# Kernel tuning notes

Hardware: AMD Instinct MI355X
Metric: run time of the kernel (lower is better)

## Reference

```python
import jax, jax.numpy as jnp
import numpy as np


def _butter1(Wn, highpass):
    """First-order Butterworth digital coefficients (bilinear transform),
    matching scipy.signal.butter(1, Wn, btype). Wn is nyquist-normalized."""
    K = jnp.tan(jnp.pi * Wn / 2.0)
    a1 = (K - 1.0) / (K + 1.0)
    if highpass:
        b0 = 1.0 / (K + 1.0)
        b1 = -b0
    else:
        b0 = K / (K + 1.0)
        b1 = b0
    return b0, b1, a1


def setup_inputs() -> dict:
    key = jax.random.key(0)
    B, T = 128, 262144
    x = jax.random.normal(key, (B, T), dtype=jnp.float32)
    return {
        "x": x,
        "center_freq": jnp.float32(1000.0),  # nn.Parameter
        "bandwidth": jnp.float32(500.0),     # nn.Parameter
        "gain": jnp.float32(1.0),            # nn.Parameter
        "sample_rate": 48000,
    }


def reference(x, center_freq, bandwidth, gain, sample_rate):
    nyq = sample_rate / 2.0
    low_wn = (center_freq - bandwidth / 2.0) / nyq
    high_wn = (center_freq + bandwidth / 2.0) / nyq
    # cascaded 1st-order highpass(low_wn) then lowpass(high_wn) = bandpass
    bh0, bh1, ah1 = _butter1(low_wn, highpass=True)
    bl0, bl1, al1 = _butter1(high_wn, highpass=False)

    xt = x.T  # [T, B] -- scan over time, vectorized over batch
    zeros = jnp.zeros((x.shape[0],), dtype=x.dtype)

    def step(carry, x_t):
        x_prev, y1_prev, y2_prev = carry
        y1 = bh0 * x_t + bh1 * x_prev - ah1 * y1_prev   # highpass stage
        y2 = bl0 * y1 + bl1 * y1_prev - al1 * y2_prev   # lowpass stage
        return (x_t, y1, y2), y2

    _, yt = jax.lax.scan(step, (zeros, zeros, zeros), xt)
    return yt.T * gain  # [B, T]
```

## Files before the change

kernel.cpp:

```cpp
#include <hip/hip_runtime.h>
#include <math.h>

#define B_    128
#define T_    262144
#define L_    16
#define NT_   256
#define WCH_  16
#define OT_   (NT_ * L_)
#define TPR_  (T_ / OT_)
#define NW_   (NT_ / 64)
#define STR_  (L_ + 1)

typedef float f32x4 __attribute__((ext_vector_type(4)));

struct Coef {
    float bh0, bh1;
    float p, q, r;
    float blc0, blc1;
};

__device__ inline void iir_step(const Coef& c, float xt, float& x_prev,
                                float& y1, float& y2) {
    float c1 = fmaf(c.bh0,  xt, c.bh1  * x_prev);
    float cx = fmaf(c.blc0, xt, c.blc1 * x_prev);
    float ny1 = fmaf(c.p, y1, c1);
    float ny2 = fmaf(c.q, y1, fmaf(c.r, y2, cx));
    y1 = ny1; y2 = ny2; x_prev = xt;
}

struct Mat { float p, q, r; };
__device__ inline Mat mat_sq(Mat m) {
    Mat o; o.p = m.p * m.p; o.q = m.q * (m.p + m.r); o.r = m.r * m.r; return o;
}
__device__ inline Mat mat_mul(Mat a, Mat b) {
    Mat o; o.p = a.p * b.p; o.q = fmaf(a.q, b.p, a.r * b.q); o.r = a.r * b.r;
    return o;
}
__device__ inline float2 mat_apply_add(Mat m, float2 v, float2 add) {
    float2 o;
    o.x = fmaf(m.p, v.x, add.x);
    o.y = fmaf(m.q, v.x, fmaf(m.r, v.y, add.y));
    return o;
}

__global__ __launch_bounds__(NT_, 8) void bp_kernel(
        const float* __restrict__ x, float* __restrict__ out,
        const float* __restrict__ cfp, const float* __restrict__ bwp,
        const float* __restrict__ gp, const int* __restrict__ srp) {
    __shared__ float  ys[NT_ * STR_];
    __shared__ float2 wagg[WCH_];
    __shared__ float2 wsagg[NW_];

    const int blk  = blockIdx.x;
    const int row  = blk >> 6;
    const int ti   = blk & (TPR_ - 1);
    const int t    = threadIdx.x;
    const int lane = t & 63;
    const int wav  = t >> 6;
    const long tile_start = (long)row * T_ + (long)ti * OT_;
    const float* xb = x + tile_start;

    const f32x4* xg = (const f32x4*)(xb + t * L_);
    f32x4 v0 = xg[0], v1 = xg[1], v2 = xg[2], v3 = xg[3];
    f32x4 w0 = (f32x4)(0.f), w1 = w0, w2 = w0, w3 = w0;
    if (t < WCH_ && ti != 0) {
        const f32x4* wg = (const f32x4*)(xb - WCH_ * L_ + t * L_);
        w0 = wg[0]; w1 = wg[1]; w2 = wg[2]; w3 = wg[3];
    }
    float xp = __shfl_up(v3.w, 1u, 64);
    if (lane == 0) xp = (ti != 0 || t != 0) ? xb[t * L_ - 1] : 0.f;

    Coef cf;
    {
        const float PIH = 1.57079632679489661923f;
        float cfv = *cfp, bwv = *bwp;
        float nyq = 0.5f * (float)(*srp);
        float K1 = tanf(PIH * (cfv - 0.5f * bwv) / nyq);
        float K2 = tanf(PIH * (cfv + 0.5f * bwv) / nyq);
        float inv1 = 1.0f / (K1 + 1.0f);
        float ah1 = (K1 - 1.0f) * inv1;
        float inv2 = 1.0f / (K2 + 1.0f);
        float bl0 = K2 * inv2;
        float al1 = (K2 - 1.0f) * inv2;
        cf.bh0 = inv1;
        cf.bh1 = -inv1;
        cf.p = -ah1;
        cf.q = bl0 - bl0 * ah1;
        cf.r = -al1;
        cf.blc0 = bl0 * inv1;
        cf.blc1 = -bl0 * inv1;
    }
    const float gain = *gp;

    Mat A  = { cf.p, cf.q, cf.r };
    Mat AL = A;
    #pragma unroll
    for (int k = 0; k < 4; ++k) AL = mat_sq(AL);
    Mat R = { 1.f, 0.f, 1.f };
    {
        Mat Mp = AL;
        unsigned b = (unsigned)lane;
        #pragma unroll
        for (int k = 0; k < 6; ++k) {
            if (b & 1u) R = mat_mul(Mp, R);
            b >>= 1u;
            if (k < 5) Mp = mat_sq(Mp);
        }
    }

    float xa[L_];
    xa[0]=v0.x; xa[1]=v0.y; xa[2]=v0.z; xa[3]=v0.w;
    xa[4]=v1.x; xa[5]=v1.y; xa[6]=v1.z; xa[7]=v1.w;
    xa[8]=v2.x; xa[9]=v2.y; xa[10]=v2.z; xa[11]=v2.w;
    xa[12]=v3.x; xa[13]=v3.y; xa[14]=v3.z; xa[15]=v3.w;
    float y2l[L_];
    float y1 = 0.f, y2 = 0.f;
    {
        float xprev = xp;
        #pragma unroll
        for (int i = 0; i < L_; ++i) {
            iir_step(cf, xa[i], xprev, y1, y2);
            y2l[i] = y2;
        }
    }

    float wxp = __shfl_up(w3.w, 1u, 64);
    if (t < WCH_) {
        float wa[L_];
        wa[0]=w0.x; wa[1]=w0.y; wa[2]=w0.z; wa[3]=w0.w;
        wa[4]=w1.x; wa[5]=w1.y; wa[6]=w1.z; wa[7]=w1.w;
        wa[8]=w2.x; wa[9]=w2.y; wa[10]=w2.z; wa[11]=w2.w;
        wa[12]=w3.x; wa[13]=w3.y; wa[14]=w3.z; wa[15]=w3.w;
        float wy1 = 0.f, wy2 = 0.f;
        float wp = (t == 0) ? 0.f : wxp;
        #pragma unroll
        for (int i = 0; i < L_; ++i) iir_step(cf, wa[i], wp, wy1, wy2);
        wagg[t] = make_float2(wy1, wy2);
    }

    float2 a = make_float2(y1, y2);
    Mat Pw = AL;
    #pragma unroll
    for (int o = 1; o < 64; o <<= 1) {
        float vx = __shfl_up(a.x, (unsigned)o, 64);
        float vy = __shfl_up(a.y, (unsigned)o, 64);
        if (lane >= o) {
            a.y = fmaf(Pw.q, vx, fmaf(Pw.r, vy, a.y));
            a.x = fmaf(Pw.p, vx, a.x);
        }
        Pw = mat_sq(Pw);
    }
    float2 ex;
    ex.x = __shfl_up(a.x, 1u, 64);
    ex.y = __shfl_up(a.y, 1u, 64);
    if (lane == 0) { ex.x = 0.f; ex.y = 0.f; }
    if (lane == 63) wsagg[wav] = a;
    __syncthreads();

    float2 S = make_float2(0.f, 0.f);
    #pragma unroll
    for (int j = 0; j < WCH_; ++j) S = mat_apply_add(AL, S, wagg[j]);
    #pragma unroll
    for (int u = 0; u < NW_ - 1; ++u)
        if (wav > u) S = mat_apply_add(Pw, S, wsagg[u]);

    float2 E = mat_apply_add(R, S, ex);

    {
        float c1 = E.x, c2 = E.y;
        float* cp = ys + t * STR_;
        #pragma unroll
        for (int i = 0; i < L_; ++i) {
            float nc1 = cf.p * c1;
            float nc2 = fmaf(cf.q, c1, cf.r * c2);
            c1 = nc1; c2 = nc2;
            cp[i] = (y2l[i] + c2) * gain;
        }
    }
    __syncthreads();

    f32x4* og = (f32x4*)(out + tile_start);
    #pragma unroll
    for (int k = 0; k < 4; ++k) {
        int F = t + NT_ * k;
        int chunk = F >> 2, pos = 4 * (F & 3);
        const float* p = ys + chunk * STR_ + pos;
        f32x4 o; o.x = p[0]; o.y = p[1]; o.z = p[2]; o.w = p[3];
        __builtin_nontemporal_store(o, og + F);
    }
}

extern "C" void kernel_launch(void* const* d_in, const int* in_sizes, int n_in,
                              void* d_out, int out_size, void* d_ws, size_t ws_size,
                              hipStream_t stream) {
    const float* x   = (const float*)d_in[0];
    const float* cfp = (const float*)d_in[1];
    const float* bwp = (const float*)d_in[2];
    const float* gp  = (const float*)d_in[3];
    const int*   srp = (const int*)d_in[4];
    float* out = (float*)d_out;

    dim3 blk(NT_), grd(B_ * TPR_);
    bp_kernel<<<grd, blk, 0, stream>>>(x, out, cfp, bwp, gp, srp);
}
```

Measured before the change: 239.1 us.

## Process two batch rows per block to interleave independent recurrences

Each block now handles the same time tile for two adjacent rows, interleaving the two independent scan chains: the serial per-thread IIR, the wave scan shuffles and the carry fix-up. This amortises per-block setup such as coefficient computation and the matrix powers, and exposes instruction-level parallelism. The cost is double the registers and LDS per block, half the grid size and a lower occupancy hint (launch bounds 8 to 4), which can reduce latency hiding for the memory-bound loads and stores.

```diff
diff --git a/kernel.cpp b/kernel.cpp
--- a/kernel.cpp
+++ b/kernel.cpp
@@ -43,32 +43,42 @@
     return o;
 }
 
-__global__ __launch_bounds__(NT_, 8) void bp_kernel(
+__global__ __launch_bounds__(NT_, 4) void bp_kernel(
         const float* __restrict__ x, float* __restrict__ out,
         const float* __restrict__ cfp, const float* __restrict__ bwp,
         const float* __restrict__ gp, const int* __restrict__ srp) {
-    __shared__ float  ys[NT_ * STR_];
-    __shared__ float2 wagg[WCH_];
-    __shared__ float2 wsagg[NW_];
+    __shared__ float  ys[2][NT_ * STR_];
+    __shared__ float2 wagg[2][WCH_];
+    __shared__ float2 wsagg[2][NW_];
 
     const int blk  = blockIdx.x;
-    const int row  = blk >> 6;
+    const int pr   = blk >> 6;
     const int ti   = blk & (TPR_ - 1);
     const int t    = threadIdx.x;
     const int lane = t & 63;
     const int wav  = t >> 6;
-    const long tile_start = (long)row * T_ + (long)ti * OT_;
-    const float* xb = x + tile_start;
-
-    const f32x4* xg = (const f32x4*)(xb + t * L_);
-    f32x4 v0 = xg[0], v1 = xg[1], v2 = xg[2], v3 = xg[3];
+    const long baseA = (long)(2 * pr)     * T_ + (long)ti * OT_;
+    const long baseB = (long)(2 * pr + 1) * T_ + (long)ti * OT_;
+    const float* xA = x + baseA;
+    const float* xB = x + baseB;
+
+    const f32x4* xgA = (const f32x4*)(xA + t * L_);
+    const f32x4* xgB = (const f32x4*)(xB + t * L_);
+    f32x4 vA0 = xgA[0], vA1 = xgA[1], vA2 = xgA[2], vA3 = xgA[3];
+    f32x4 vB0 = xgB[0], vB1 = xgB[1], vB2 = xgB[2], vB3 = xgB[3];
     f32x4 w0 = (f32x4)(0.f), w1 = w0, w2 = w0, w3 = w0;
-    if (t < WCH_ && ti != 0) {
-        const f32x4* wg = (const f32x4*)(xb - WCH_ * L_ + t * L_);
+    const int wt = t & 15;
+    if (t < 32 && ti != 0) {
+        const float* wb = (t < 16 ? xA : xB) - WCH_ * L_ + wt * L_;
+        const f32x4* wg = (const f32x4*)wb;
         w0 = wg[0]; w1 = wg[1]; w2 = wg[2]; w3 = wg[3];
     }
-    float xp = __shfl_up(v3.w, 1u, 64);
-    if (lane == 0) xp = (ti != 0 || t != 0) ? xb[t * L_ - 1] : 0.f;
+    float xpA = __shfl_up(vA3.w, 1u, 64);
+    float xpB = __shfl_up(vB3.w, 1u, 64);
+    if (lane == 0) {
+        xpA = (ti != 0 || t != 0) ? xA[t * L_ - 1] : 0.f;
+        xpB = (ti != 0 || t != 0) ? xB[t * L_ - 1] : 0.f;
+    }
 
     Coef cf;
     {
@@ -108,85 +118,114 @@
         }
     }
 
-    float xa[L_];
-    xa[0]=v0.x; xa[1]=v0.y; xa[2]=v0.z; xa[3]=v0.w;
-    xa[4]=v1.x; xa[5]=v1.y; xa[6]=v1.z; xa[7]=v1.w;
-    xa[8]=v2.x; xa[9]=v2.y; xa[10]=v2.z; xa[11]=v2.w;
-    xa[12]=v3.x; xa[13]=v3.y; xa[14]=v3.z; xa[15]=v3.w;
-    float y2l[L_];
-    float y1 = 0.f, y2 = 0.f;
-    {
-        float xprev = xp;
+    float aA_[L_], aB_[L_];
+    aA_[0]=vA0.x; aA_[1]=vA0.y; aA_[2]=vA0.z; aA_[3]=vA0.w;
+    aA_[4]=vA1.x; aA_[5]=vA1.y; aA_[6]=vA1.z; aA_[7]=vA1.w;
+    aA_[8]=vA2.x; aA_[9]=vA2.y; aA_[10]=vA2.z; aA_[11]=vA2.w;
+    aA_[12]=vA3.x; aA_[13]=vA3.y; aA_[14]=vA3.z; aA_[15]=vA3.w;
+    aB_[0]=vB0.x; aB_[1]=vB0.y; aB_[2]=vB0.z; aB_[3]=vB0.w;
+    aB_[4]=vB1.x; aB_[5]=vB1.y; aB_[6]=vB1.z; aB_[7]=vB1.w;
+    aB_[8]=vB2.x; aB_[9]=vB2.y; aB_[10]=vB2.z; aB_[11]=vB2.w;
+    aB_[12]=vB3.x; aB_[13]=vB3.y; aB_[14]=vB3.z; aB_[15]=vB3.w;
+    float y2lA[L_], y2lB[L_];
+    float y1A = 0.f, y2A = 0.f, y1B = 0.f, y2B = 0.f;
+    {
+        float xprevA = xpA, xprevB = xpB;
         #pragma unroll
         for (int i = 0; i < L_; ++i) {
-            iir_step(cf, xa[i], xprev, y1, y2);
-            y2l[i] = y2;
+            iir_step(cf, aA_[i], xprevA, y1A, y2A);
+            iir_step(cf, aB_[i], xprevB, y1B, y2B);
+            y2lA[i] = y2A;
+            y2lB[i] = y2B;
         }
     }
 
     float wxp = __shfl_up(w3.w, 1u, 64);
-    if (t < WCH_) {
+    if (t < 32) {
         float wa[L_];
         wa[0]=w0.x; wa[1]=w0.y; wa[2]=w0.z; wa[3]=w0.w;
         wa[4]=w1.x; wa[5]=w1.y; wa[6]=w1.z; wa[7]=w1.w;
         wa[8]=w2.x; wa[9]=w2.y; wa[10]=w2.z; wa[11]=w2.w;
         wa[12]=w3.x; wa[13]=w3.y; wa[14]=w3.z; wa[15]=w3.w;
         float wy1 = 0.f, wy2 = 0.f;
-        float wp = (t == 0) ? 0.f : wxp;
+        float wp = (wt == 0) ? 0.f : wxp;
         #pragma unroll
         for (int i = 0; i < L_; ++i) iir_step(cf, wa[i], wp, wy1, wy2);
-        wagg[t] = make_float2(wy1, wy2);
-    }
-
-    float2 a = make_float2(y1, y2);
+        wagg[t >> 4][wt] = make_float2(wy1, wy2);
+    }
+
+    float2 aA = make_float2(y1A, y2A);
+    float2 aB = make_float2(y1B, y2B);
     Mat Pw = AL;
     #pragma unroll
     for (int o = 1; o < 64; o <<= 1) {
-        float vx = __shfl_up(a.x, (unsigned)o, 64);
-        float vy = __shfl_up(a.y, (unsigned)o, 64);
+        float vxA = __shfl_up(aA.x, (unsigned)o, 64);
+        float vyA = __shfl_up(aA.y, (unsigned)o, 64);
+        float vxB = __shfl_up(aB.x, (unsigned)o, 64);
+        float vyB = __shfl_up(aB.y, (unsigned)o, 64);
         if (lane >= o) {
-            a.y = fmaf(Pw.q, vx, fmaf(Pw.r, vy, a.y));
-            a.x = fmaf(Pw.p, vx, a.x);
+            aA.y = fmaf(Pw.q, vxA, fmaf(Pw.r, vyA, aA.y));
+            aA.x = fmaf(Pw.p, vxA, aA.x);
+            aB.y = fmaf(Pw.q, vxB, fmaf(Pw.r, vyB, aB.y));
+            aB.x = fmaf(Pw.p, vxB, aB.x);
         }
         Pw = mat_sq(Pw);
     }
-    float2 ex;
-    ex.x = __shfl_up(a.x, 1u, 64);
-    ex.y = __shfl_up(a.y, 1u, 64);
-    if (lane == 0) { ex.x = 0.f; ex.y = 0.f; }
-    if (lane == 63) wsagg[wav] = a;
+    float2 exA, exB;
+    exA.x = __shfl_up(aA.x, 1u, 64);
+    exA.y = __shfl_up(aA.y, 1u, 64);
+    exB.x = __shfl_up(aB.x, 1u, 64);
+    exB.y = __shfl_up(aB.y, 1u, 64);
+    if (lane == 0) { exA.x = exA.y = exB.x = exB.y = 0.f; }
+    if (lane == 63) { wsagg[0][wav] = aA; wsagg[1][wav] = aB; }
     __syncthreads();
 
-    float2 S = make_float2(0.f, 0.f);
-    #pragma unroll
-    for (int j = 0; j < WCH_; ++j) S = mat_apply_add(AL, S, wagg[j]);
-    #pragma unroll
-    for (int u = 0; u < NW_ - 1; ++u)
-        if (wav > u) S = mat_apply_add(Pw, S, wsagg[u]);
-
-    float2 E = mat_apply_add(R, S, ex);
-
-    {
-        float c1 = E.x, c2 = E.y;
-        float* cp = ys + t * STR_;
+    float2 SA = make_float2(0.f, 0.f), SB = SA;
+    #pragma unroll
+    for (int j = 0; j < WCH_; ++j) {
+        SA = mat_apply_add(AL, SA, wagg[0][j]);
+        SB = mat_apply_add(AL, SB, wagg[1][j]);
+    }
+    #pragma unroll
+    for (int u = 0; u < NW_ - 1; ++u) {
+        if (wav > u) {
+            SA = mat_apply_add(Pw, SA, wsagg[0][u]);
+            SB = mat_apply_add(Pw, SB, wsagg[1][u]);
+        }
+    }
+
+    float2 EA = mat_apply_add(R, SA, exA);
+    float2 EB = mat_apply_add(R, SB, exB);
+
+    {
+        float c1A = EA.x, c2A = EA.y, c1B = EB.x, c2B = EB.y;
+        float* cpA = ys[0] + t * STR_;
+        float* cpB = ys[1] + t * STR_;
         #pragma unroll
         for (int i = 0; i < L_; ++i) {
-            float nc1 = cf.p * c1;
-            float nc2 = fmaf(cf.q, c1, cf.r * c2);
-            c1 = nc1; c2 = nc2;
-            cp[i] = (y2l[i] + c2) * gain;
+            float n1A = cf.p * c1A;
+            float n2A = fmaf(cf.q, c1A, cf.r * c2A);
+            float n1B = cf.p * c1B;
+            float n2B = fmaf(cf.q, c1B, cf.r * c2B);
+            c1A = n1A; c2A = n2A; c1B = n1B; c2B = n2B;
+            cpA[i] = (y2lA[i] + c2A) * gain;
+            cpB[i] = (y2lB[i] + c2B) * gain;
         }
     }
     __syncthreads();
 
-    f32x4* og = (f32x4*)(out + tile_start);
+    f32x4* ogA = (f32x4*)(out + baseA);
+    f32x4* ogB = (f32x4*)(out + baseB);
     #pragma unroll
     for (int k = 0; k < 4; ++k) {
         int F = t + NT_ * k;
         int chunk = F >> 2, pos = 4 * (F & 3);
-        const float* p = ys + chunk * STR_ + pos;
-        f32x4 o; o.x = p[0]; o.y = p[1]; o.z = p[2]; o.w = p[3];
-        __builtin_nontemporal_store(o, og + F);
+        const float* pA = ys[0] + chunk * STR_ + pos;
+        const float* pB = ys[1] + chunk * STR_ + pos;
+        f32x4 oA; oA.x = pA[0]; oA.y = pA[1]; oA.z = pA[2]; oA.w = pA[3];
+        f32x4 oB; oB.x = pB[0]; oB.y = pB[1]; oB.z = pB[2]; oB.w = pB[3];
+        __builtin_nontemporal_store(oA, ogA + F);
+        __builtin_nontemporal_store(oB, ogB + F);
     }
 }
 
@@ -200,6 +239,6 @@
     const int*   srp = (const int*)d_in[4];
     float* out = (float*)d_out;
 
-    dim3 blk(NT_), grd(B_ * TPR_);
+    dim3 blk(NT_), grd((B_ / 2) * TPR_);
     bp_kernel<<<grd, blk, 0, stream>>>(x, out, cfp, bwp, gp, srp);
 }
```

After: 239.6 us. No clear change (+0.2%).

## Process four consecutive tiles per block with carried state and prefetch

Applied to the files above, without the earlier changes.

Each block now handles four consecutive tiles of a row. The inter-tile state is carried exactly across tiles, so only the first tile pays for the warm-up window recompute. The next tile's input is prefetched with nontemporal loads while the current tile's scan runs. The grid shrinks fourfold and launch bounds drop to 4 waves per SIMD. Fewer blocks and serial tiles per block reduce parallelism, and the prefetch raises register pressure.

```diff
diff --git a/kernel.cpp b/kernel.cpp
--- a/kernel.cpp
+++ b/kernel.cpp
@@ -10,6 +10,8 @@
 #define TPR_  (T_ / OT_)
 #define NW_   (NT_ / 64)
 #define STR_  (L_ + 1)
+#define GPB_  4
+#define NBLK_ ((B_ * TPR_) / GPB_)
 
 typedef float f32x4 __attribute__((ext_vector_type(4)));
 
@@ -43,7 +45,7 @@
     return o;
 }
 
-__global__ __launch_bounds__(NT_, 8) void bp_kernel(
+__global__ __launch_bounds__(NT_, 4) void bp_kernel(
         const float* __restrict__ x, float* __restrict__ out,
         const float* __restrict__ cfp, const float* __restrict__ bwp,
         const float* __restrict__ gp, const int* __restrict__ srp) {
@@ -52,23 +54,32 @@
     __shared__ float2 wsagg[NW_];
 
     const int blk  = blockIdx.x;
-    const int row  = blk >> 6;
-    const int ti   = blk & (TPR_ - 1);
     const int t    = threadIdx.x;
     const int lane = t & 63;
     const int wav  = t >> 6;
-    const long tile_start = (long)row * T_ + (long)ti * OT_;
-    const float* xb = x + tile_start;
-
-    const f32x4* xg = (const f32x4*)(xb + t * L_);
-    f32x4 v0 = xg[0], v1 = xg[1], v2 = xg[2], v3 = xg[3];
+
+    const int tid0 = blk * GPB_;
+    const int row  = tid0 >> 6;
+    const int ti0  = tid0 & (TPR_ - 1);
+    const long base0 = (long)row * T_ + (long)ti0 * OT_;
+
+    {
+        const float* xb = x + base0;
+        (void)xb;
+    }
+    const float* xb0 = x + base0;
+    const f32x4* xg0 = (const f32x4*)(xb0 + t * L_);
+    f32x4 v0 = __builtin_nontemporal_load(xg0 + 0);
+    f32x4 v1 = __builtin_nontemporal_load(xg0 + 1);
+    f32x4 v2 = __builtin_nontemporal_load(xg0 + 2);
+    f32x4 v3 = __builtin_nontemporal_load(xg0 + 3);
     f32x4 w0 = (f32x4)(0.f), w1 = w0, w2 = w0, w3 = w0;
-    if (t < WCH_ && ti != 0) {
-        const f32x4* wg = (const f32x4*)(xb - WCH_ * L_ + t * L_);
+    if (t < WCH_ && ti0 != 0) {
+        const f32x4* wg = (const f32x4*)(xb0 - WCH_ * L_ + t * L_);
         w0 = wg[0]; w1 = wg[1]; w2 = wg[2]; w3 = wg[3];
     }
-    float xp = __shfl_up(v3.w, 1u, 64);
-    if (lane == 0) xp = (ti != 0 || t != 0) ? xb[t * L_ - 1] : 0.f;
+    float lxp = 0.f;
+    if (lane == 0 && (ti0 != 0 || t != 0)) lxp = xb0[t * L_ - 1];
 
     Coef cf;
     {
@@ -108,85 +119,122 @@
         }
     }
 
-    float xa[L_];
-    xa[0]=v0.x; xa[1]=v0.y; xa[2]=v0.z; xa[3]=v0.w;
-    xa[4]=v1.x; xa[5]=v1.y; xa[6]=v1.z; xa[7]=v1.w;
-    xa[8]=v2.x; xa[9]=v2.y; xa[10]=v2.z; xa[11]=v2.w;
-    xa[12]=v3.x; xa[13]=v3.y; xa[14]=v3.z; xa[15]=v3.w;
-    float y2l[L_];
-    float y1 = 0.f, y2 = 0.f;
-    {
-        float xprev = xp;
-        #pragma unroll
-        for (int i = 0; i < L_; ++i) {
-            iir_step(cf, xa[i], xprev, y1, y2);
-            y2l[i] = y2;
-        }
-    }
-
-    float wxp = __shfl_up(w3.w, 1u, 64);
-    if (t < WCH_) {
-        float wa[L_];
-        wa[0]=w0.x; wa[1]=w0.y; wa[2]=w0.z; wa[3]=w0.w;
-        wa[4]=w1.x; wa[5]=w1.y; wa[6]=w1.z; wa[7]=w1.w;
-        wa[8]=w2.x; wa[9]=w2.y; wa[10]=w2.z; wa[11]=w2.w;
-        wa[12]=w3.x; wa[13]=w3.y; wa[14]=w3.z; wa[15]=w3.w;
-        float wy1 = 0.f, wy2 = 0.f;
-        float wp = (t == 0) ? 0.f : wxp;
-        #pragma unroll
-        for (int i = 0; i < L_; ++i) iir_step(cf, wa[i], wp, wy1, wy2);
-        wagg[t] = make_float2(wy1, wy2);
-    }
-
-    float2 a = make_float2(y1, y2);
-    Mat Pw = AL;
+    float2 Scar = make_float2(0.f, 0.f);
+
     #pragma unroll
-    for (int o = 1; o < 64; o <<= 1) {
-        float vx = __shfl_up(a.x, (unsigned)o, 64);
-        float vy = __shfl_up(a.y, (unsigned)o, 64);
-        if (lane >= o) {
-            a.y = fmaf(Pw.q, vx, fmaf(Pw.r, vy, a.y));
-            a.x = fmaf(Pw.p, vx, a.x);
-        }
-        Pw = mat_sq(Pw);
-    }
-    float2 ex;
-    ex.x = __shfl_up(a.x, 1u, 64);
-    ex.y = __shfl_up(a.y, 1u, 64);
-    if (lane == 0) { ex.x = 0.f; ex.y = 0.f; }
-    if (lane == 63) wsagg[wav] = a;
-    __syncthreads();
-
-    float2 S = make_float2(0.f, 0.f);
-    #pragma unroll
-    for (int j = 0; j < WCH_; ++j) S = mat_apply_add(AL, S, wagg[j]);
-    #pragma unroll
-    for (int u = 0; u < NW_ - 1; ++u)
-        if (wav > u) S = mat_apply_add(Pw, S, wsagg[u]);
-
-    float2 E = mat_apply_add(R, S, ex);
-
-    {
-        float c1 = E.x, c2 = E.y;
-        float* cp = ys + t * STR_;
-        #pragma unroll
-        for (int i = 0; i < L_; ++i) {
-            float nc1 = cf.p * c1;
-            float nc2 = fmaf(cf.q, c1, cf.r * c2);
-            c1 = nc1; c2 = nc2;
-            cp[i] = (y2l[i] + c2) * gain;
-        }
-    }
-    __syncthreads();
-
-    f32x4* og = (f32x4*)(out + tile_start);
-    #pragma unroll
-    for (int k = 0; k < 4; ++k) {
-        int F = t + NT_ * k;
-        int chunk = F >> 2, pos = 4 * (F & 3);
-        const float* p = ys + chunk * STR_ + pos;
-        f32x4 o; o.x = p[0]; o.y = p[1]; o.z = p[2]; o.w = p[3];
-        __builtin_nontemporal_store(o, og + F);
+    for (int g = 0; g < GPB_; ++g) {
+        const long base = base0 + (long)g * OT_;
+
+        float xp = __shfl_up(v3.w, 1u, 64);
+        if (lane == 0) xp = lxp;
+
+        float xa[L_];
+        xa[0]=v0.x; xa[1]=v0.y; xa[2]=v0.z; xa[3]=v0.w;
+        xa[4]=v1.x; xa[5]=v1.y; xa[6]=v1.z; xa[7]=v1.w;
+        xa[8]=v2.x; xa[9]=v2.y; xa[10]=v2.z; xa[11]=v2.w;
+        xa[12]=v3.x; xa[13]=v3.y; xa[14]=v3.z; xa[15]=v3.w;
+        float y2l[L_];
+        float y1 = 0.f, y2 = 0.f;
+        {
+            float xprev = xp;
+            #pragma unroll
+            for (int i = 0; i < L_; ++i) {
+                iir_step(cf, xa[i], xprev, y1, y2);
+                y2l[i] = y2;
+            }
+        }
+
+        if (g == 0) {
+            float wxp = __shfl_up(w3.w, 1u, 64);
+            if (t < WCH_) {
+                float wa[L_];
+                wa[0]=w0.x; wa[1]=w0.y; wa[2]=w0.z; wa[3]=w0.w;
+                wa[4]=w1.x; wa[5]=w1.y; wa[6]=w1.z; wa[7]=w1.w;
+                wa[8]=w2.x; wa[9]=w2.y; wa[10]=w2.z; wa[11]=w2.w;
+                wa[12]=w3.x; wa[13]=w3.y; wa[14]=w3.z; wa[15]=w3.w;
+                float wy1 = 0.f, wy2 = 0.f;
+                float wp = (t == 0) ? 0.f : wxp;
+                #pragma unroll
+                for (int i = 0; i < L_; ++i) iir_step(cf, wa[i], wp, wy1, wy2);
+                wagg[t] = make_float2(wy1, wy2);
+            }
+        }
+
+        if (g + 1 < GPB_) {
+            const float* nxb = x + base + OT_;
+            const f32x4* nxg = (const f32x4*)(nxb + t * L_);
+            v0 = __builtin_nontemporal_load(nxg + 0);
+            v1 = __builtin_nontemporal_load(nxg + 1);
+            v2 = __builtin_nontemporal_load(nxg + 2);
+            v3 = __builtin_nontemporal_load(nxg + 3);
+            if (lane == 0) lxp = nxb[t * L_ - 1];
+        }
+
+        float2 a = make_float2(y1, y2);
+        Mat Pw = AL;
+        #pragma unroll
+        for (int o = 1; o < 64; o <<= 1) {
+            float vx = __shfl_up(a.x, (unsigned)o, 64);
+            float vy = __shfl_up(a.y, (unsigned)o, 64);
+            if (lane >= o) {
+                a.y = fmaf(Pw.q, vx, fmaf(Pw.r, vy, a.y));
+                a.x = fmaf(Pw.p, vx, a.x);
+            }
+            Pw = mat_sq(Pw);
+        }
+        float2 ex;
+        ex.x = __shfl_up(a.x, 1u, 64);
+        ex.y = __shfl_up(a.y, 1u, 64);
+        if (lane == 0) { ex.x = 0.f; ex.y = 0.f; }
+        if (lane == 63) wsagg[wav] = a;
+        __syncthreads();
+
+        float2 S;
+        if (g == 0) {
+            S = make_float2(0.f, 0.f);
+            #pragma unroll
+            for (int j = 0; j < WCH_; ++j) S = mat_apply_add(AL, S, wagg[j]);
+        } else {
+            S = Scar;
+        }
+
+        {
+            float2 Stot = wsagg[0];
+            #pragma unroll
+            for (int u = 1; u < NW_; ++u) Stot = mat_apply_add(Pw, Stot, wsagg[u]);
+            Mat P2 = mat_sq(Pw);
+            Mat P4 = mat_sq(P2);
+            Scar = mat_apply_add(P4, S, Stot);
+        }
+
+        float2 Sw = S;
+        #pragma unroll
+        for (int u = 0; u < NW_ - 1; ++u)
+            if (wav > u) Sw = mat_apply_add(Pw, Sw, wsagg[u]);
+        float2 E = mat_apply_add(R, Sw, ex);
+
+        {
+            float c1 = E.x, c2 = E.y;
+            float* cp = ys + t * STR_;
+            #pragma unroll
+            for (int i = 0; i < L_; ++i) {
+                float nc1 = cf.p * c1;
+                float nc2 = fmaf(cf.q, c1, cf.r * c2);
+                c1 = nc1; c2 = nc2;
+                cp[i] = (y2l[i] + c2) * gain;
+            }
+        }
+        __syncthreads();
+
+        f32x4* og = (f32x4*)(out + base);
+        #pragma unroll
+        for (int k = 0; k < 4; ++k) {
+            int F = t + NT_ * k;
+            int chunk = F >> 2, pos = 4 * (F & 3);
+            const float* p = ys + chunk * STR_ + pos;
+            f32x4 o; o.x = p[0]; o.y = p[1]; o.z = p[2]; o.w = p[3];
+            __builtin_nontemporal_store(o, og + F);
+        }
     }
 }
 
@@ -200,6 +248,6 @@
     const int*   srp = (const int*)d_in[4];
     float* out = (float*)d_out;
 
-    dim3 blk(NT_), grd(B_ * TPR_);
+    dim3 blk(NT_), grd(NBLK_);
     bp_kernel<<<grd, blk, 0, stream>>>(x, out, cfp, bwp, gp, srp);
 }
```

Measured after the change: 243.1 us. Within noise of the previous version (+1.7%).
